# Optimization experiments

Hardware: AMD Instinct MI355X
Metric: run time of the kernel (lower is better)

The kernel has to match this reference:

```python
import jax, jax.numpy as jnp
import numpy as np

N, E, IN, H, OUT = 100000, 1600000, 128, 128, 64


def setup_inputs() -> dict:
    key = jax.random.key(0)
    ks = jax.random.split(key, 7)
    x = jax.random.normal(ks[0], (N, IN), dtype=jnp.float32)
    edge_index = jax.random.randint(ks[1], (2, E), 0, N, dtype=jnp.int32)
    # Glorot-style scaled params (PyG SAGEConv: lin_l has bias, lin_r does not)
    s1 = 1.0 / np.sqrt(IN)
    s2 = 1.0 / np.sqrt(H)
    W1_l = jax.random.normal(ks[2], (H, IN), dtype=jnp.float32) * s1
    W1_r = jax.random.normal(ks[3], (H, IN), dtype=jnp.float32) * s1
    b1 = jnp.zeros((H,), dtype=jnp.float32)
    W2_l = jax.random.normal(ks[4], (OUT, H), dtype=jnp.float32) * s2
    W2_r = jax.random.normal(ks[5], (OUT, H), dtype=jnp.float32) * s2
    b2 = jnp.zeros((OUT,), dtype=jnp.float32)
    return {"x": x, "W1_l": W1_l, "W1_r": W1_r, "b1": b1,
            "W2_l": W2_l, "W2_r": W2_r, "b2": b2, "edge_index": edge_index}


def _sage_conv(x, edge_index, W_l, W_r, b):
    # mean-aggregate source-node features at target nodes, then linear + root term
    src, dst = edge_index[0], edge_index[1]
    n = x.shape[0]
    msgs = x[src]                                                   # [E, d]
    agg = jax.ops.segment_sum(msgs, dst, num_segments=n)            # [N, d]
    deg = jax.ops.segment_sum(jnp.ones((src.shape[0],), x.dtype), dst, num_segments=n)
    mean = agg / jnp.clip(deg, 1.0)[:, None]                        # zero-deg nodes stay 0
    return mean @ W_l.T + b + x @ W_r.T


def reference(x, W1_l, W1_r, b1, W2_l, W2_r, b2, edge_index):
    h = _sage_conv(x, edge_index, W1_l, W1_r, b1)
    h = jax.nn.relu(h)  # dropout p=0.0 -> identity
    out = _sage_conv(h, edge_index, W2_l, W2_r, b2)
    return out
```

## Files before the change

kernel.cpp:

```cpp
#include <hip/hip_runtime.h>


typedef unsigned int uint32;
typedef short bf16x4 __attribute__((ext_vector_type(4)));
typedef short bf16x8 __attribute__((ext_vector_type(8)));
typedef float f32x16 __attribute__((ext_vector_type(16)));
typedef float f32x2 __attribute__((ext_vector_type(2)));

#define PSTR 264

__device__ __forceinline__ uint32 pack_bf16_rne(float a, float b) {
    uint32 ua = __float_as_uint(a);
    uint32 ub = __float_as_uint(b);
    uint32 ra = (ua + 0x7fffu + ((ua >> 16) & 1u)) >> 16;
    uint32 rb = (ub + 0x7fffu + ((ub >> 16) & 1u)) >> 16;
    return ra | (rb << 16);
}
__device__ __forceinline__ float bf_lo(uint32 v) { return __uint_as_float(v << 16); }
__device__ __forceinline__ float bf_hi(uint32 v) { return __uint_as_float(v & 0xffff0000u); }

__device__ __forceinline__ short rne16(float v, float* back) {
    uint32 u = __float_as_uint(v);
    uint32 r = (u + 0x7fffu + ((u >> 16) & 1u)) >> 16;
    *back = __uint_as_float(r << 16);
    return (short)r;
}

__global__ void k_prepcount(const float* __restrict__ x, uint32* __restrict__ xb,
                            long n4,
                            const float* __restrict__ W1l, const float* __restrict__ W1r,
                            const float* __restrict__ W2l, const float* __restrict__ W2r,
                            short* __restrict__ W1pH, short* __restrict__ W1pL,
                            short* __restrict__ W2pH, short* __restrict__ W2pL,
                            const int* __restrict__ ei, int E, int NB,
                            int* __restrict__ bucket_cnt, int prep_blocks) {
    __shared__ int hist[512];
    int t = threadIdx.x;
    if ((int)blockIdx.x >= prep_blocks) {
        int bb = (int)blockIdx.x - prep_blocks;
        for (int i = t; i < NB; i += 256) hist[i] = 0;
        __syncthreads();
        int stride = 256 * 256;
        for (int e = bb * 256 + t; e < E; e += stride)
            atomicAdd(&hist[ei[E + e] >> 8], 1);
        __syncthreads();
        for (int i = t; i < NB; i += 256) {
            int c = hist[i];
            if (c) atomicAdd(&bucket_cnt[i], c);
        }
        return;
    }
    long i = (long)blockIdx.x * blockDim.x + t;
    float back;
    if (i < n4) {
        float4 v = ((const float4*)x)[i];
        short h0 = rne16(v.x, &back);
        short h1 = rne16(v.y, &back);
        short h2 = rne16(v.z, &back);
        short h3 = rne16(v.w, &back);
        uint2 o;
        o.x = (uint32)(unsigned short)h0 | ((uint32)(unsigned short)h1 << 16);
        o.y = (uint32)(unsigned short)h2 | ((uint32)(unsigned short)h3 << 16);
        ((uint2*)xb)[i] = o;
        return;
    }
    int i2 = (int)(i - n4);
    if (i2 < 32768) {
        int j = i2 >> 8, k = i2 & 255;
        float v = (k < 128) ? W1l[j * 128 + k] : W1r[j * 128 + k - 128];
        float hb;
        short hs = rne16(v, &hb);
        short ls = rne16(v - hb, &back);
        int idx = (k >> 3) * 1024 + j * 8 + (k & 7);
        W1pH[idx] = hs;
        W1pL[idx] = ls;
    } else if (i2 < 32768 + 16384) {
        int i3 = i2 - 32768;
        int j = i3 >> 7, k = i3 & 127;
        float v = (j < 64) ? W2l[j * 128 + k] : W2r[(j - 64) * 128 + k];
        float hb;
        short hs = rne16(v, &hb);
        short ls = rne16(v - hb, &back);
        int idx = (k >> 3) * 1024 + j * 8 + (k & 7);
        W2pH[idx] = hs;
        W2pL[idx] = ls;
    }
}

__global__ void k_bscatter(const int* __restrict__ ei, int E, int NB,
                           const int* __restrict__ bcnt, int* __restrict__ bcur,
                           uint32* __restrict__ eb) {
    __shared__ int sc[512];
    __shared__ int hist[512];
    __shared__ int basev[512];
    int t = threadIdx.x;
    int c0 = (t < NB) ? bcnt[t] : 0;
    int c1 = (t + 256 < NB) ? bcnt[t + 256] : 0;
    sc[t] = c0;
    sc[t + 256] = c1;
    hist[t] = 0;
    hist[t + 256] = 0;
    __syncthreads();
    for (int o = 1; o < 512; o <<= 1) {
        int a0 = (t >= o) ? sc[t - o] : 0;
        int a1 = (t + 256 >= o) ? sc[t + 256 - o] : 0;
        __syncthreads();
        sc[t] += a0;
        sc[t + 256] += a1;
        __syncthreads();
    }
    int stride = gridDim.x * 256;
    for (int e = blockIdx.x * 256 + t; e < E; e += stride)
        atomicAdd(&hist[ei[E + e] >> 8], 1);
    __syncthreads();
    {
        int c = hist[t];
        if (t < NB) basev[t] = (sc[t] - c0) + (c ? atomicAdd(&bcur[t], c) : 0);
        hist[t] = 0;
        int i1 = t + 256;
        int c2 = hist[i1];
        if (i1 < NB) basev[i1] = (sc[i1] - c1) + (c2 ? atomicAdd(&bcur[i1], c2) : 0);
        hist[i1] = 0;
    }
    __syncthreads();
    for (int e = blockIdx.x * 256 + t; e < E; e += stride) {
        int d = ei[E + e];
        int b = d >> 8;
        int r = atomicAdd(&hist[b], 1);
        eb[basev[b] + r] = ((uint32)(d & 255) << 24) | (uint32)ei[e];
    }
}

__global__ void k_bfinal(const uint32* __restrict__ eb,
                         const int* __restrict__ bcnt,
                         int* __restrict__ row_ptr, int* __restrict__ col,
                         int N, int E, int NB) {
    __shared__ int sc[512];
    __shared__ int deg[256];
    __shared__ int scn[256];
    __shared__ int cur[256];
    int b = blockIdx.x;
    int t = threadIdx.x;
    sc[t] = (t < NB) ? bcnt[t] : 0;
    sc[t + 256] = (t + 256 < NB) ? bcnt[t + 256] : 0;
    deg[t] = 0;
    __syncthreads();
    for (int o = 1; o < 512; o <<= 1) {
        int a0 = (t >= o) ? sc[t - o] : 0;
        int a1 = (t + 256 >= o) ? sc[t + 256 - o] : 0;
        __syncthreads();
        sc[t] += a0;
        sc[t + 256] += a1;
        __syncthreads();
    }
    int beg = (b > 0) ? sc[b - 1] : 0;
    int end = sc[b];
    for (int e = beg + t; e < end; e += 256)
        atomicAdd(&deg[eb[e] >> 24], 1);
    __syncthreads();
    int v = deg[t];
    scn[t] = v;
    __syncthreads();
    for (int o = 1; o < 256; o <<= 1) {
        int u = (t >= o) ? scn[t - o] : 0;
        __syncthreads();
        scn[t] += u;
        __syncthreads();
    }
    int ex = scn[t] - v;
    int node = b * 256 + t;
    if (node < N) row_ptr[node] = beg + ex;
    if (b == gridDim.x - 1 && t == 0) row_ptr[N] = E;
    cur[t] = ex;
    __syncthreads();
    for (int e = beg + t; e < end; e += 256) {
        uint32 u = eb[e];
        int r = atomicAdd(&cur[u >> 24], 1);
        col[beg + r] = (int)(u & 0xFFFFFFu);
    }
}


__global__ __launch_bounds__(256, 4) void k_fused(
        const int* __restrict__ rp, const int* __restrict__ col,
        const uint32* __restrict__ xb,
        const short* __restrict__ W1pH, const short* __restrict__ W1pL,
        const short* __restrict__ W2pH, const short* __restrict__ W2pL,
        const float* __restrict__ b1, const float* __restrict__ b2,
        unsigned short* __restrict__ hl, float* __restrict__ hr, int N) {
    __shared__ short smH[16 * PSTR];
    __shared__ short smL[16 * PSTR];
    int t = threadIdx.x;
    int w = t >> 6, lane = t & 63;
    int g = lane >> 4, f = lane & 15;
    int node0 = blockIdx.x * 32;
    const uint4* xb4 = (const uint4*)xb;

    int base = node0 + 8 * w;
    int rpi = base + lane;
    if (rpi > N) rpi = N;
    int rpv = rp[rpi];

    uint4 cvv[8];
#pragma unroll
    for (int i = 0; i < 8; i++) {
        int bi = __shfl(rpv, i);
        cvv[i] = *(const uint4*)(col + bi + 4 * g);
    }
    uint4 p0 = {}, p1 = {}, p2 = {}, p3 = {};
    {
        int b0 = __builtin_amdgcn_readfirstlane(__shfl(rpv, 0));
        int e0 = __builtin_amdgcn_readfirstlane(__shfl(rpv, 1));
        if (e0 - b0 >= 16) {
            uint4 cvp = cvv[0];
            p0 = xb4[(size_t)cvp.x * 16 + f];
            p1 = xb4[(size_t)cvp.y * 16 + f];
            p2 = xb4[(size_t)cvp.z * 16 + f];
            p3 = xb4[(size_t)cvp.w * 16 + f];
        }
    }

#pragma unroll
    for (int i = 0; i < 8; i++) {
        int lr = 8 * w + i;
        int beg = __builtin_amdgcn_readfirstlane(__shfl(rpv, i));
        int end = __builtin_amdgcn_readfirstlane(__shfl(rpv, i + 1));
        f32x2 sA[4];
#pragma unroll
        for (int j = 0; j < 4; j++) sA[j] = (f32x2){0.f, 0.f};

#define ACC_RAW(v)                                                      \
    { sA[0] += (f32x2){bf_lo(v.x), __uint_as_float(v.x)};               \
      sA[1] += (f32x2){bf_lo(v.y), __uint_as_float(v.y)};               \
      sA[2] += (f32x2){bf_lo(v.z), __uint_as_float(v.z)};               \
      sA[3] += (f32x2){bf_lo(v.w), __uint_as_float(v.w)}; }

        int e = beg;
        bool has16 = (e + 16 <= end);
        uint4 v0, v1, v2, v3;
        if (has16) { v0 = p0; v1 = p1; v2 = p2; v3 = p3; }
        if (i < 7) {
            int nb = __builtin_amdgcn_readfirstlane(__shfl(rpv, i + 1));
            int ne = __builtin_amdgcn_readfirstlane(__shfl(rpv, i + 2));
            if (ne - nb >= 16) {
                uint4 cvp = cvv[i + 1];
                p0 = xb4[(size_t)cvp.x * 16 + f];
                p1 = xb4[(size_t)cvp.y * 16 + f];
                p2 = xb4[(size_t)cvp.z * 16 + f];
                p3 = xb4[(size_t)cvp.w * 16 + f];
            }
        }
        if (has16) {
            uint4 cv = *(const uint4*)(col + e + 16 + 4 * g);
            ACC_RAW(v0); ACC_RAW(v1); ACC_RAW(v2); ACC_RAW(v3);
            e += 16;
            while (e + 16 <= end) {
                uint4 w0 = xb4[(size_t)cv.x * 16 + f];
                uint4 w1 = xb4[(size_t)cv.y * 16 + f];
                uint4 w2 = xb4[(size_t)cv.z * 16 + f];
                uint4 w3 = xb4[(size_t)cv.w * 16 + f];
                uint4 cvn = *(const uint4*)(col + e + 16 + 4 * g);
                ACC_RAW(w0); ACC_RAW(w1); ACC_RAW(w2); ACC_RAW(w3);
                e += 16;
                cv = cvn;
            }
        }
        for (; e + 8 <= end; e += 8) {
            uint2 cv2 = *(const uint2*)(col + e + 2 * g);
            uint4 u0 = xb4[(size_t)cv2.x * 16 + f];
            uint4 u1 = xb4[(size_t)cv2.y * 16 + f];
            ACC_RAW(u0); ACC_RAW(u1);
        }
        int rem = end - e;
        if (2 * g < rem) {
            uint4 u0 = xb4[(size_t)col[e + 2 * g] * 16 + f];
            ACC_RAW(u0);
        }
        if (2 * g + 1 < rem) {
            uint4 u0 = xb4[(size_t)col[e + 2 * g + 1] * 16 + f];
            ACC_RAW(u0);
        }
#undef ACC_RAW
#pragma unroll
        for (int p = 0; p < 4; p++) {
            sA[p].x += __shfl_xor(sA[p].x, 16);
            sA[p].y += __shfl_xor(sA[p].y, 16);
            sA[p].x += __shfl_xor(sA[p].x, 32);
            sA[p].y += __shfl_xor(sA[p].y, 32);
        }
        float inv = 1.0f / (float)max(end - beg, 1);
        float m0 = sA[g].x * inv, m1 = sA[g].y * inv;
        float b_;
        short h0 = rne16(m0, &b_);
        float bk0 = b_;
        short l0 = rne16(m0 - bk0, &b_);
        short h1 = rne16(m1, &b_);
        float bk1 = b_;
        short l1 = rne16(m1 - bk1, &b_);
        uint32 H = (uint32)(unsigned short)h0 | ((uint32)(unsigned short)h1 << 16);
        uint32 L = (uint32)(unsigned short)l0 | ((uint32)(unsigned short)l1 << 16);
        *(uint32*)&smH[f * PSTR + lr * 8 + 2 * g] = H;
        *(uint32*)&smL[f * PSTR + lr * 8 + 2 * g] = L;
    }
    __syncthreads();

    int m = lane & 31, hh = lane >> 5;
    int mynode = node0 + m;
    const short* xbs = (const short*)xb;
    f32x16 acc;
#pragma unroll
    for (int r = 0; r < 16; r++) acc[r] = 0.f;
#pragma unroll
    for (int kc = 0; kc < 8; kc++) {
        int c = 2 * kc + hh;
        bf16x8 bH = *(const bf16x8*)&smH[c * PSTR + m * 8];
        bf16x8 bL = *(const bf16x8*)&smL[c * PSTR + m * 8];
        bf16x8 xH = *(const bf16x8*)(xbs + (size_t)mynode * 128 + c * 8);
        bf16x8 aH1 = *(const bf16x8*)(W1pH + c * 1024 + (32 * w + m) * 8);
        bf16x8 aL1 = *(const bf16x8*)(W1pL + c * 1024 + (32 * w + m) * 8);
        bf16x8 aH2 = *(const bf16x8*)(W1pH + (16 + c) * 1024 + (32 * w + m) * 8);
        bf16x8 aL2 = *(const bf16x8*)(W1pL + (16 + c) * 1024 + (32 * w + m) * 8);
        acc = __builtin_amdgcn_mfma_f32_32x32x16_bf16(aH1, bH, acc, 0, 0, 0);
        acc = __builtin_amdgcn_mfma_f32_32x32x16_bf16(aL1, bH, acc, 0, 0, 0);
        acc = __builtin_amdgcn_mfma_f32_32x32x16_bf16(aH1, bL, acc, 0, 0, 0);
        acc = __builtin_amdgcn_mfma_f32_32x32x16_bf16(aH2, xH, acc, 0, 0, 0);
        acc = __builtin_amdgcn_mfma_f32_32x32x16_bf16(aL2, xH, acc, 0, 0, 0);
    }

    uint2 oh[4], ol[4];
#pragma unroll
    for (int rg = 0; rg < 4; rg++) {
        int j0 = 32 * w + 8 * rg + 4 * hh;
        float4 bv = *(const float4*)(b1 + j0);
        float bb[4] = {bv.x, bv.y, bv.z, bv.w};
        short hs[4], ls[4];
#pragma unroll
        for (int q = 0; q < 4; q++) {
            float v = fmaxf(acc[4 * rg + q] + bb[q], 0.f);
            float back;
            hs[q] = rne16(v, &back);
            ls[q] = rne16(v - back, &back);
        }
        oh[rg].x = (uint32)(unsigned short)hs[0] | ((uint32)(unsigned short)hs[1] << 16);
        oh[rg].y = (uint32)(unsigned short)hs[2] | ((uint32)(unsigned short)hs[3] << 16);
        ol[rg].x = (uint32)(unsigned short)ls[0] | ((uint32)(unsigned short)ls[1] << 16);
        ol[rg].y = (uint32)(unsigned short)ls[2] | ((uint32)(unsigned short)ls[3] << 16);
    }
    __syncthreads();
#pragma unroll
    for (int rg = 0; rg < 4; rg++) {
        int idx = (4 * w + rg) * PSTR + m * 8 + 4 * hh;
        *(uint2*)&smH[idx] = oh[rg];
        *(uint2*)&smL[idx] = ol[rg];
    }
    __syncthreads();

#pragma unroll
    for (int r = 0; r < 16; r++) acc[r] = 0.f;
#pragma unroll
    for (int kc = 0; kc < 8; kc++) {
        int c = 2 * kc + hh;
        bf16x8 bH = *(const bf16x8*)&smH[c * PSTR + m * 8];
        bf16x8 bL = *(const bf16x8*)&smL[c * PSTR + m * 8];
        bf16x8 aH = *(const bf16x8*)(W2pH + c * 1024 + (32 * w + m) * 8);
        bf16x8 aL = *(const bf16x8*)(W2pL + c * 1024 + (32 * w + m) * 8);
        acc = __builtin_amdgcn_mfma_f32_32x32x16_bf16(aH, bH, acc, 0, 0, 0);
        acc = __builtin_amdgcn_mfma_f32_32x32x16_bf16(aL, bH, acc, 0, 0, 0);
        acc = __builtin_amdgcn_mfma_f32_32x32x16_bf16(aH, bL, acc, 0, 0, 0);
    }
    if (mynode >= N) return;
    if (w < 2) {
#pragma unroll
        for (int rg = 0; rg < 4; rg++) {
            int j0 = 32 * w + 8 * rg + 4 * hh;
            uint2 o;
            o.x = pack_bf16_rne(acc[4 * rg + 0], acc[4 * rg + 1]);
            o.y = pack_bf16_rne(acc[4 * rg + 2], acc[4 * rg + 3]);
            *(uint2*)&hl[(size_t)mynode * 64 + j0] = o;
        }
    } else {
#pragma unroll
        for (int rg = 0; rg < 4; rg++) {
            int j0 = 32 * (w - 2) + 8 * rg + 4 * hh;
            float4 bv = *(const float4*)(b2 + j0);
            float4 o;
            o.x = acc[4 * rg + 0] + bv.x;
            o.y = acc[4 * rg + 1] + bv.y;
            o.z = acc[4 * rg + 2] + bv.z;
            o.w = acc[4 * rg + 3] + bv.w;
            *(float4*)&hr[(size_t)mynode * 64 + j0] = o;
        }
    }
}


__global__ void k_agg_out(const int* __restrict__ rp, const int* __restrict__ col,
                          const uint32* __restrict__ hl, const float* __restrict__ hr,
                          float* __restrict__ out, int N) {
    int node = blockIdx.x * 4 + (threadIdx.x >> 6);
    if (node >= N) return;
    node = __builtin_amdgcn_readfirstlane(node);
    int lane = threadIdx.x & 63;
    int g = lane >> 3;
    int f = lane & 7;
    int beg = rp[node], end = rp[node + 1];
    const uint4* hl4 = (const uint4*)hl;
    f32x2 sA[4];
#pragma unroll
    for (int j = 0; j < 4; j++) sA[j] = (f32x2){0.f, 0.f};

#define ACC_MSK(v)                                          \
    { sA[0] += (f32x2){bf_lo(v.x), bf_hi(v.x)};             \
      sA[1] += (f32x2){bf_lo(v.y), bf_hi(v.y)};             \
      sA[2] += (f32x2){bf_lo(v.z), bf_hi(v.z)};             \
      sA[3] += (f32x2){bf_lo(v.w), bf_hi(v.w)}; }

    uint2 cv = *(const uint2*)(col + beg + 2 * g);
    int e = beg;
    for (; e + 16 <= end; e += 16) {
        uint2 cvn = *(const uint2*)(col + e + 16 + 2 * g);
        uint4 v0 = hl4[(size_t)cv.x * 8 + f];
        uint4 v1 = hl4[(size_t)cv.y * 8 + f];
        ACC_MSK(v0); ACC_MSK(v1);
        cv = cvn;
    }
    for (; e + 8 <= end; e += 8) {
        uint4 v0 = hl4[(size_t)col[e + g] * 8 + f];
        ACC_MSK(v0);
    }
    int rem = end - e;
    if (g < rem) {
        uint4 v0 = hl4[(size_t)col[e + g] * 8 + f];
        ACC_MSK(v0);
    }
#undef ACC_MSK
#pragma unroll
    for (int p = 0; p < 4; p++) {
        sA[p].x += __shfl_xor(sA[p].x, 8);
        sA[p].y += __shfl_xor(sA[p].y, 8);
        sA[p].x += __shfl_xor(sA[p].x, 16);
        sA[p].y += __shfl_xor(sA[p].y, 16);
        sA[p].x += __shfl_xor(sA[p].x, 32);
        sA[p].y += __shfl_xor(sA[p].y, 32);
    }
    if (g == 0) {
        float inv = 1.0f / (float)max(end - beg, 1);
        const float* hrp = hr + (size_t)node * 64 + f * 8;
        float4 h0 = *(const float4*)(hrp);
        float4 h1 = *(const float4*)(hrp + 4);
        float4 o0, o1;
        o0.x = sA[0].x * inv + h0.x;
        o0.y = sA[0].y * inv + h0.y;
        o0.z = sA[1].x * inv + h0.z;
        o0.w = sA[1].y * inv + h0.w;
        o1.x = sA[2].x * inv + h1.x;
        o1.y = sA[2].y * inv + h1.y;
        o1.z = sA[3].x * inv + h1.z;
        o1.w = sA[3].y * inv + h1.w;
        float* op = out + (size_t)node * 64 + f * 8;
        *(float4*)(op) = o0;
        *(float4*)(op + 4) = o1;
    }
}

extern "C" void kernel_launch(void* const* d_in, const int* in_sizes, int n_in,
                              void* d_out, int out_size, void* d_ws, size_t ws_size,
                              hipStream_t stream) {
    const float* x   = (const float*)d_in[0];
    const float* W1l = (const float*)d_in[1];
    const float* W1r = (const float*)d_in[2];
    const float* b1  = (const float*)d_in[3];
    const float* W2l = (const float*)d_in[4];
    const float* W2r = (const float*)d_in[5];
    const float* b2  = (const float*)d_in[6];
    const int*   ei  = (const int*)d_in[7];
    int N = in_sizes[0] / 128;
    int E = in_sizes[7] / 2;
    int NB = (N + 255) >> 8;
    int mb = (N + 31) / 32;
    int Np = ((N + 127) / 128) * 128;
    float* out = (float*)d_out;

    char* w = (char*)d_ws;
    size_t off = 0;
    auto alloc = [&](size_t bytes) -> char* {
        char* p = w + off;
        off += (bytes + 255) & ~(size_t)255;
        return p;
    };
    int*   row_ptr = (int*)alloc((size_t)(N + 1) * 4);
    int*   bwork   = (int*)alloc((size_t)2 * (NB + 1) * 4);
    short* W1pH    = (short*)alloc(32768 * 2);
    short* W1pL    = (short*)alloc(32768 * 2);
    short* W2pH    = (short*)alloc(16384 * 2);
    short* W2pL    = (short*)alloc(16384 * 2);
    int*   col     = (int*)alloc((size_t)E * 4);
    uint32* xb     = (uint32*)alloc((size_t)Np * 64 * 4);
    float*  hr     = (float*)alloc((size_t)Np * 64 * 4);
    unsigned short* hl = (unsigned short*)alloc((size_t)N * 64 * 2);
    int* bcnt = bwork;
    int* bcur = bwork + (NB + 1);
    uint32* eb = (uint32*)hl;

    hipMemsetAsync(bwork, 0, (size_t)2 * (NB + 1) * 4, stream);
    long n4 = (long)N * 32;
    long prep_items = n4 + 32768 + 16384;
    int prep_blocks = (int)((prep_items + 255) / 256);
    k_prepcount<<<prep_blocks + 256, 256, 0, stream>>>(
        x, xb, n4, W1l, W1r, W2l, W2r, W1pH, W1pL, W2pH, W2pL,
        ei, E, NB, bcnt, prep_blocks);
    k_bscatter<<<128, 256, 0, stream>>>(ei, E, NB, bcnt, bcur, eb);
    k_bfinal<<<NB, 256, 0, stream>>>(eb, bcnt, row_ptr, col, N, E, NB);

    k_fused<<<mb, 256, 0, stream>>>(row_ptr, col, xb, W1pH, W1pL, W2pH, W2pL,
                                    b1, b2, hl, hr, N);
    int ab = (N + 3) / 4;
    k_agg_out<<<ab, 256, 0, stream>>>(row_ptr, col, (const uint32*)hl, hr, out, N);
}
```

Before: 340.4 us.

## Drop cross-row prefetch in layer-1 gather; remap layer-2 gather to 16 lanes per row

In the fused layer-1 kernel, the software pipelining that preloaded column indices for all eight rows and prefetched the next row's first 16 neighbour features is removed in favour of a plain unrolled 16-edge loop. This cuts register pressure, which may raise occupancy, at the cost of exposing load latency. In the layer-2 aggregation kernel, each 64-lane wave now uses 16 lanes per row with 8-byte loads instead of 8 lanes with 16-byte loads, gathering four edges per iteration instead of eight. This shortens the cross-lane reduction and the per-lane accumulator set but issues smaller memory transactions.

```diff
diff --git a/kernel.cpp b/kernel.cpp
--- a/kernel.cpp
+++ b/kernel.cpp
@@ -201,26 +201,6 @@
     if (rpi > N) rpi = N;
     int rpv = rp[rpi];
 
-    uint4 cvv[8];
-#pragma unroll
-    for (int i = 0; i < 8; i++) {
-        int bi = __shfl(rpv, i);
-        cvv[i] = *(const uint4*)(col + bi + 4 * g);
-    }
-    uint4 p0 = {}, p1 = {}, p2 = {}, p3 = {};
-    {
-        int b0 = __builtin_amdgcn_readfirstlane(__shfl(rpv, 0));
-        int e0 = __builtin_amdgcn_readfirstlane(__shfl(rpv, 1));
-        if (e0 - b0 >= 16) {
-            uint4 cvp = cvv[0];
-            p0 = xb4[(size_t)cvp.x * 16 + f];
-            p1 = xb4[(size_t)cvp.y * 16 + f];
-            p2 = xb4[(size_t)cvp.z * 16 + f];
-            p3 = xb4[(size_t)cvp.w * 16 + f];
-        }
-    }
-
-#pragma unroll
     for (int i = 0; i < 8; i++) {
         int lr = 8 * w + i;
         int beg = __builtin_amdgcn_readfirstlane(__shfl(rpv, i));
@@ -236,49 +216,28 @@
       sA[3] += (f32x2){bf_lo(v.w), __uint_as_float(v.w)}; }
 
         int e = beg;
-        bool has16 = (e + 16 <= end);
-        uint4 v0, v1, v2, v3;
-        if (has16) { v0 = p0; v1 = p1; v2 = p2; v3 = p3; }
-        if (i < 7) {
-            int nb = __builtin_amdgcn_readfirstlane(__shfl(rpv, i + 1));
-            int ne = __builtin_amdgcn_readfirstlane(__shfl(rpv, i + 2));
-            if (ne - nb >= 16) {
-                uint4 cvp = cvv[i + 1];
-                p0 = xb4[(size_t)cvp.x * 16 + f];
-                p1 = xb4[(size_t)cvp.y * 16 + f];
-                p2 = xb4[(size_t)cvp.z * 16 + f];
-                p3 = xb4[(size_t)cvp.w * 16 + f];
-            }
-        }
-        if (has16) {
-            uint4 cv = *(const uint4*)(col + e + 16 + 4 * g);
+        for (; e + 16 <= end; e += 16) {
+            uint4 cv = *(const uint4*)(col + e + 4 * g);
+            uint4 v0 = xb4[(size_t)cv.x * 16 + f];
+            uint4 v1 = xb4[(size_t)cv.y * 16 + f];
+            uint4 v2 = xb4[(size_t)cv.z * 16 + f];
+            uint4 v3 = xb4[(size_t)cv.w * 16 + f];
             ACC_RAW(v0); ACC_RAW(v1); ACC_RAW(v2); ACC_RAW(v3);
-            e += 16;
-            while (e + 16 <= end) {
-                uint4 w0 = xb4[(size_t)cv.x * 16 + f];
-                uint4 w1 = xb4[(size_t)cv.y * 16 + f];
-                uint4 w2 = xb4[(size_t)cv.z * 16 + f];
-                uint4 w3 = xb4[(size_t)cv.w * 16 + f];
-                uint4 cvn = *(const uint4*)(col + e + 16 + 4 * g);
-                ACC_RAW(w0); ACC_RAW(w1); ACC_RAW(w2); ACC_RAW(w3);
-                e += 16;
-                cv = cvn;
-            }
         }
         for (; e + 8 <= end; e += 8) {
-            uint2 cv2 = *(const uint2*)(col + e + 2 * g);
-            uint4 u0 = xb4[(size_t)cv2.x * 16 + f];
-            uint4 u1 = xb4[(size_t)cv2.y * 16 + f];
-            ACC_RAW(u0); ACC_RAW(u1);
+            uint2 cv = *(const uint2*)(col + e + 2 * g);
+            uint4 v0 = xb4[(size_t)cv.x * 16 + f];
+            uint4 v1 = xb4[(size_t)cv.y * 16 + f];
+            ACC_RAW(v0); ACC_RAW(v1);
         }
         int rem = end - e;
         if (2 * g < rem) {
-            uint4 u0 = xb4[(size_t)col[e + 2 * g] * 16 + f];
-            ACC_RAW(u0);
+            uint4 v0 = xb4[(size_t)col[e + 2 * g] * 16 + f];
+            ACC_RAW(v0);
         }
         if (2 * g + 1 < rem) {
-            uint4 u0 = xb4[(size_t)col[e + 2 * g + 1] * 16 + f];
-            ACC_RAW(u0);
+            uint4 v0 = xb4[(size_t)col[e + 2 * g + 1] * 16 + f];
+            ACC_RAW(v0);
         }
 #undef ACC_RAW
 #pragma unroll
@@ -401,43 +360,39 @@
     if (node >= N) return;
     node = __builtin_amdgcn_readfirstlane(node);
     int lane = threadIdx.x & 63;
-    int g = lane >> 3;
-    int f = lane & 7;
+    int g = lane >> 4;
+    int f = lane & 15;
     int beg = rp[node], end = rp[node + 1];
-    const uint4* hl4 = (const uint4*)hl;
-    f32x2 sA[4];
-#pragma unroll
-    for (int j = 0; j < 4; j++) sA[j] = (f32x2){0.f, 0.f};
+    const uint2* hl2 = (const uint2*)hl;
+    f32x2 sA[2];
+    sA[0] = (f32x2){0.f, 0.f};
+    sA[1] = (f32x2){0.f, 0.f};
 
 #define ACC_MSK(v)                                          \
     { sA[0] += (f32x2){bf_lo(v.x), bf_hi(v.x)};             \
-      sA[1] += (f32x2){bf_lo(v.y), bf_hi(v.y)};             \
-      sA[2] += (f32x2){bf_lo(v.z), bf_hi(v.z)};             \
-      sA[3] += (f32x2){bf_lo(v.w), bf_hi(v.w)}; }
-
-    uint2 cv = *(const uint2*)(col + beg + 2 * g);
+      sA[1] += (f32x2){bf_lo(v.y), bf_hi(v.y)}; }
+
     int e = beg;
     for (; e + 16 <= end; e += 16) {
-        uint2 cvn = *(const uint2*)(col + e + 16 + 2 * g);
-        uint4 v0 = hl4[(size_t)cv.x * 8 + f];
-        uint4 v1 = hl4[(size_t)cv.y * 8 + f];
-        ACC_MSK(v0); ACC_MSK(v1);
-        cv = cvn;
-    }
-    for (; e + 8 <= end; e += 8) {
-        uint4 v0 = hl4[(size_t)col[e + g] * 8 + f];
+        uint4 cv = *(const uint4*)(col + e + 4 * g);
+        uint2 v0 = hl2[(size_t)cv.x * 16 + f];
+        uint2 v1 = hl2[(size_t)cv.y * 16 + f];
+        uint2 v2 = hl2[(size_t)cv.z * 16 + f];
+        uint2 v3 = hl2[(size_t)cv.w * 16 + f];
+        ACC_MSK(v0); ACC_MSK(v1); ACC_MSK(v2); ACC_MSK(v3);
+    }
+    for (; e + 4 <= end; e += 4) {
+        uint2 v0 = hl2[(size_t)col[e + g] * 16 + f];
         ACC_MSK(v0);
     }
     int rem = end - e;
     if (g < rem) {
-        uint4 v0 = hl4[(size_t)col[e + g] * 8 + f];
+        uint2 v0 = hl2[(size_t)col[e + g] * 16 + f];
         ACC_MSK(v0);
     }
 #undef ACC_MSK
 #pragma unroll
-    for (int p = 0; p < 4; p++) {
-        sA[p].x += __shfl_xor(sA[p].x, 8);
-        sA[p].y += __shfl_xor(sA[p].y, 8);
+    for (int p = 0; p < 2; p++) {
         sA[p].x += __shfl_xor(sA[p].x, 16);
         sA[p].y += __shfl_xor(sA[p].y, 16);
         sA[p].x += __shfl_xor(sA[p].x, 32);
@@ -445,21 +400,15 @@
     }
     if (g == 0) {
         float inv = 1.0f / (float)max(end - beg, 1);
-        const float* hrp = hr + (size_t)node * 64 + f * 8;
+        const float* hrp = hr + (size_t)node * 64 + f * 4;
         float4 h0 = *(const float4*)(hrp);
-        float4 h1 = *(const float4*)(hrp + 4);
-        float4 o0, o1;
+        float4 o0;
         o0.x = sA[0].x * inv + h0.x;
         o0.y = sA[0].y * inv + h0.y;
         o0.z = sA[1].x * inv + h0.z;
         o0.w = sA[1].y * inv + h0.w;
-        o1.x = sA[2].x * inv + h1.x;
-        o1.y = sA[2].y * inv + h1.y;
-        o1.z = sA[3].x * inv + h1.z;
-        o1.w = sA[3].y * inv + h1.w;
-        float* op = out + (size_t)node * 64 + f * 8;
+        float* op = out + (size_t)node * 64 + f * 4;
         *(float4*)(op) = o0;
-        *(float4*)(op + 4) = o1;
     }
 }
 
```

Measured after the change: 323.0 us. -5.1%, faster.
